# Kernel optimization log

Hardware: AMD Instinct MI355X
Metric: run time of the kernel (lower is better)

Reference implementation:

```python
import jax, jax.numpy as jnp
import numpy as np

B, S, D, H = 4, 2048, 1024, 16
HD = D // H  # head_dim = 64

def setup_inputs() -> dict:
    key = jax.random.key(0)
    ks = jax.random.split(key, 6)
    scale = 1.0 / np.sqrt(D)
    x = jax.random.normal(ks[0], (B, S, D), dtype=jnp.float32)
    Wq = jax.random.normal(ks[1], (D, D), dtype=jnp.float32) * scale
    Wk = jax.random.normal(ks[2], (D, D), dtype=jnp.float32) * scale
    Wv = jax.random.normal(ks[3], (D, D), dtype=jnp.float32) * scale
    Wo = jax.random.normal(ks[4], (D, D), dtype=jnp.float32) * scale
    z = jnp.zeros((D,), dtype=jnp.float32)
    return {"x": x, "Wq": Wq, "bq": z, "Wk": Wk, "bk": z, "Wv": Wv, "bv": z, "Wo": Wo, "bo": z}

def reference(x, Wq, bq, Wk, bk, Wv, bv, Wo, bo):
    b, s, d = x.shape
    hd = d // H
    def split_heads(t):
        return t.reshape(b, s, H, hd).swapaxes(1, 2)  # [B,H,S,hd]
    q = split_heads(x @ Wq + bq)
    k = split_heads(x @ Wk + bk)
    v = split_heads(x @ Wv + bv)
    logits = jnp.einsum('bhqd,bhkd->bhqk', q, k) / jnp.sqrt(jnp.asarray(hd, x.dtype))
    attn = jax.nn.softmax(logits, axis=-1)
    vals = jnp.einsum('bhqk,bhkd->bhqd', attn, v)
    vals = vals.swapaxes(1, 2).reshape(b, s, d)
    return vals @ Wo + bo
```

## Files before the change

kernel.cpp:

```cpp
#include <hip/hip_runtime.h>
#include <hip/hip_bf16.h>
#include <cstdint>
#include <cstddef>


typedef __attribute__((ext_vector_type(8))) short short8;
typedef __attribute__((ext_vector_type(8))) unsigned short ushort8;
typedef __attribute__((ext_vector_type(4))) unsigned short ushort4v;
typedef __attribute__((ext_vector_type(4))) float floatx4;

#define LOG2E 1.44269504088896340736f
#define QSCALE (0.125f * LOG2E)

__device__ __forceinline__ unsigned short f2bf(float f) {
  union { float f; unsigned int u; } c; c.f = f;
  return (unsigned short)((c.u + 0x7fffu + ((c.u >> 16) & 1u)) >> 16);
}

__device__ __forceinline__ unsigned int pack_bf16(float a, float b) {
  unsigned int ua = __builtin_bit_cast(unsigned int, a) + 0x8000u;
  unsigned int ub = __builtin_bit_cast(unsigned int, b) + 0x8000u;
  return __builtin_amdgcn_perm(ub, ua, 0x07060302);
}

__device__ __forceinline__ float fexp2(float x) {
#if __HIP_DEVICE_COMPILE__
  return __builtin_amdgcn_exp2f(x);
#else
  return x;
#endif
}

__device__ __forceinline__ void gl_lds16(const void* g, void* l) {
  __builtin_amdgcn_global_load_lds((__attribute__((address_space(1))) void*)g,
                                   (__attribute__((address_space(3))) void*)l, 16, 0, 0);
}

__global__ __launch_bounds__(256) void cast_x_kernel(const float* __restrict__ x,
                                                     unsigned short* __restrict__ xb, int n4) {
  int i = blockIdx.x * 256 + threadIdx.x;
  if (i >= n4) return;
  float4 v = ((const float4*)x)[i];
  ushort4v o;
  o.x = f2bf(v.x); o.y = f2bf(v.y); o.z = f2bf(v.z); o.w = f2bf(v.w);
  ((ushort4v*)xb)[i] = o;
}

__global__ __launch_bounds__(256) void transpose_w_kernel(
    const float* __restrict__ Wq, const float* __restrict__ Wk,
    const float* __restrict__ Wv, const float* __restrict__ Wo,
    unsigned short* __restrict__ Wqkv_t, unsigned short* __restrict__ Wo_t) {
  __shared__ float tile[32][33];
  const int which = blockIdx.z;
  const float* src = (which == 0) ? Wq : (which == 1) ? Wk : (which == 2) ? Wv : Wo;
  unsigned short* dst = (which == 3) ? Wo_t : (Wqkv_t + (size_t)which * 1024 * 1024);
  const int bn = blockIdx.x * 32;
  const int bk = blockIdx.y * 32;
  const int tx = threadIdx.x & 31, ty = threadIdx.x >> 5;
#pragma unroll
  for (int r = 0; r < 32; r += 8)
    tile[ty + r][tx] = src[(size_t)(bk + ty + r) * 1024 + bn + tx];
  __syncthreads();
#pragma unroll
  for (int r = 0; r < 32; r += 8)
    dst[(size_t)(bn + ty + r) * 1024 + bk + tx] = f2bf(tile[tx][ty + r]);
}

template <int MODE>
__global__ __launch_bounds__(256, 3) void gemm_bt(
    const unsigned short* __restrict__ A, const unsigned short* __restrict__ Bt,
    int M, int N, int K,
    const float* __restrict__ bias0, const float* __restrict__ bias1,
    const float* __restrict__ bias2,
    unsigned short* __restrict__ outQ, unsigned short* __restrict__ outK,
    unsigned short* __restrict__ outVt, float* __restrict__ outF) {
  __shared__ unsigned short As[128 * 32];
  __shared__ unsigned short Bs[128 * 32];

  const int tid = threadIdx.x;
  const int lane = tid & 63;
  const int wid = tid >> 6;
  const int wm = wid >> 1, wn = wid & 1;
  const int l15 = lane & 15, q4 = lane >> 4;
  const int bm = blockIdx.x * 128, bn = blockIdx.y * 128;

  const int rowL = lane >> 2;
  const int segL = (lane & 3) * 16;

  const char* Ab = (const char*)A;
  const char* Bb = (const char*)Bt;
  const size_t strideA = (size_t)K * 2;

  floatx4 acc[4][4] = {};

  for (int k0 = 0; k0 < K; k0 += 32) {
    __syncthreads();
#pragma unroll
    for (int c0 = 0; c0 < 2; ++c0) {
      const int c = wid * 2 + c0;
      gl_lds16(Ab + (size_t)(bm + c * 16 + rowL) * strideA + (size_t)k0 * 2 + segL,
               &As[c * 512]);
      gl_lds16(Bb + (size_t)(bn + c * 16 + rowL) * strideA + (size_t)k0 * 2 + segL,
               &Bs[c * 512]);
    }
    __syncthreads();

    short8 af[4], bfr[4];
#pragma unroll
    for (int i = 0; i < 4; ++i)
      af[i] = *(const short8*)&As[(wm * 64 + i * 16 + l15) * 32 + q4 * 8];
#pragma unroll
    for (int j = 0; j < 4; ++j)
      bfr[j] = *(const short8*)&Bs[(wn * 64 + j * 16 + l15) * 32 + q4 * 8];
#pragma unroll
    for (int i = 0; i < 4; ++i)
#pragma unroll
      for (int j = 0; j < 4; ++j)
        acc[i][j] = __builtin_amdgcn_mfma_f32_16x16x32_bf16(af[i], bfr[j], acc[i][j], 0, 0, 0);
  }

#pragma unroll
  for (int i = 0; i < 4; ++i) {
    const int row0 = bm + wm * 64 + i * 16 + q4 * 4;
#pragma unroll
    for (int j = 0; j < 4; ++j) {
      const int gn = bn + wn * 64 + j * 16 + l15;
      if (MODE == 0) {
        const int b = row0 >> 11, s0 = row0 & 2047;
        const int region = gn >> 10, d = gn & 1023;
        const int h = d >> 6, hd = d & 63;
        const size_t bh = (size_t)(b * 16 + h);
        if (region == 0) {
          const float bb = bias0[d];
#pragma unroll
          for (int r = 0; r < 4; ++r)
            outQ[(bh * 2048 + s0 + r) * 64 + hd] = f2bf((acc[i][j][r] + bb) * QSCALE);
        } else if (region == 1) {
          const float bb = bias1[d];
#pragma unroll
          for (int r = 0; r < 4; ++r)
            outK[(bh * 2048 + s0 + r) * 64 + hd] = f2bf(acc[i][j][r] + bb);
        } else {
          const float bb = bias2[d];
          ushort4v pk;
#pragma unroll
          for (int r = 0; r < 4; ++r) pk[r] = f2bf(acc[i][j][r] + bb);
          *(ushort4v*)&outVt[(bh * 64 + hd) * 2048 + s0] = pk;
        }
      } else {
        const float bb = bias0[gn];
#pragma unroll
        for (int r = 0; r < 4; ++r)
          outF[(size_t)(row0 + r) * N + gn] = acc[i][j][r] + bb;
      }
    }
  }
}

__global__ __launch_bounds__(256, 2) void flash_attn(
    const unsigned short* __restrict__ Q, const unsigned short* __restrict__ Kg,
    const unsigned short* __restrict__ Vt, unsigned short* __restrict__ Oout) {
  __shared__ unsigned short Ks[2][64 * 72];
  __shared__ unsigned short Vs[2][64 * 72];

  const int tid = threadIdx.x, lane = tid & 63, wid = tid >> 6;
  const int l15 = lane & 15, q4 = lane >> 4;
  const int bh = blockIdx.y;
  const int bb = bh >> 4, hh = bh & 15;
  const int q0 = blockIdx.x * 256;
  const size_t base = (size_t)bh * 2048 * 64;

  short8 qf[4][2];
#pragma unroll
  for (int s = 0; s < 4; ++s) {
    const unsigned short* qrow = Q + base + (size_t)(q0 + s * 64 + wid * 16 + l15) * 64;
    qf[s][0] = *(const short8*)(qrow + q4 * 8);
    qf[s][1] = *(const short8*)(qrow + 32 + q4 * 8);
  }

  const int sr = tid >> 2;
  const int sg = (tid & 3) * 16;
  const int loc = sr & 31;
  const int ph = (loc >> 4) & 1, pq = (loc >> 2) & 3, pr = loc & 3;
  const int gp = (sr & 32) + pq * 8 + ph * 4 + pr;
  const unsigned short* Kbase = Kg + base + (size_t)gp * 64 + sg;
  const unsigned short* Vbase = Vt + base + (size_t)sr * 2048 + sg;

  ushort8 kr0, kr1, vr0, vr1;
  kr0 = *(const ushort8*)Kbase;       kr1 = *(const ushort8*)(Kbase + 8);
  vr0 = *(const ushort8*)Vbase;       vr1 = *(const ushort8*)(Vbase + 8);
  *(ushort8*)&Ks[0][sr * 72 + sg] = kr0;  *(ushort8*)&Ks[0][sr * 72 + sg + 8] = kr1;
  *(ushort8*)&Vs[0][sr * 72 + sg] = vr0;  *(ushort8*)&Vs[0][sr * 72 + sg + 8] = vr1;
  kr0 = *(const ushort8*)(Kbase + 4096);  kr1 = *(const ushort8*)(Kbase + 4104);
  vr0 = *(const ushort8*)(Vbase + 64);    vr1 = *(const ushort8*)(Vbase + 72);

  floatx4 oacc[4][4] = {};
  float lsum[4] = {0.f, 0.f, 0.f, 0.f};

  for (int it = 0; it < 32; ++it) {
    const int cur = it & 1;
    __syncthreads();
    if (it < 31) {
      *(ushort8*)&Ks[cur ^ 1][sr * 72 + sg] = kr0;
      *(ushort8*)&Ks[cur ^ 1][sr * 72 + sg + 8] = kr1;
      *(ushort8*)&Vs[cur ^ 1][sr * 72 + sg] = vr0;
      *(ushort8*)&Vs[cur ^ 1][sr * 72 + sg + 8] = vr1;
    }
    if (it < 30) {
      const unsigned short* kp = Kbase + (size_t)(it + 2) * 4096;
      const unsigned short* vp = Vbase + (size_t)(it + 2) * 64;
      kr0 = *(const ushort8*)kp;       kr1 = *(const ushort8*)(kp + 8);
      vr0 = *(const ushort8*)vp;       vr1 = *(const ushort8*)(vp + 8);
    }

    short8 pf[4][2];
#pragma unroll
    for (int c = 0; c < 2; ++c) {
      floatx4 sc[4][2] = {};
#pragma unroll
      for (int tt = 0; tt < 2; ++tt) {
        const int t = 2 * c + tt;
        const unsigned short* krow = &Ks[cur][(t * 16 + l15) * 72];
        short8 kf0 = *(const short8*)(krow + q4 * 8);
        short8 kf1 = *(const short8*)(krow + 32 + q4 * 8);
#pragma unroll
        for (int s = 0; s < 4; ++s) {
          sc[s][tt] = __builtin_amdgcn_mfma_f32_16x16x32_bf16(kf0, qf[s][0], sc[s][tt], 0, 0, 0);
          sc[s][tt] = __builtin_amdgcn_mfma_f32_16x16x32_bf16(kf1, qf[s][1], sc[s][tt], 0, 0, 0);
        }
      }
#pragma unroll
      for (int s = 0; s < 4; ++s) {
        float e0 = fexp2(sc[s][0][0]), e1 = fexp2(sc[s][0][1]);
        float e2 = fexp2(sc[s][0][2]), e3 = fexp2(sc[s][0][3]);
        float e4 = fexp2(sc[s][1][0]), e5 = fexp2(sc[s][1][1]);
        float e6 = fexp2(sc[s][1][2]), e7 = fexp2(sc[s][1][3]);
        lsum[s] += ((e0 + e1) + (e2 + e3)) + ((e4 + e5) + (e6 + e7));
        union { unsigned int u[4]; short8 v; } cv;
        cv.u[0] = pack_bf16(e0, e1); cv.u[1] = pack_bf16(e2, e3);
        cv.u[2] = pack_bf16(e4, e5); cv.u[3] = pack_bf16(e6, e7);
        pf[s][c] = cv.v;
      }
    }

#pragma unroll
    for (int t = 0; t < 4; ++t) {
      const unsigned short* vrow = &Vs[cur][(t * 16 + l15) * 72 + q4 * 8];
      short8 vf0 = *(const short8*)vrow;
      short8 vf1 = *(const short8*)(vrow + 32);
#pragma unroll
      for (int s = 0; s < 4; ++s) {
        oacc[s][t] = __builtin_amdgcn_mfma_f32_16x16x32_bf16(vf0, pf[s][0], oacc[s][t], 0, 0, 0);
        oacc[s][t] = __builtin_amdgcn_mfma_f32_16x16x32_bf16(vf1, pf[s][1], oacc[s][t], 0, 0, 0);
      }
    }
  }

#pragma unroll
  for (int s = 0; s < 4; ++s) {
    float l = lsum[s];
    l += __shfl_xor(l, 16);
    l += __shfl_xor(l, 32);
    const float inv = 1.0f / l;
    const int srow = q0 + s * 64 + wid * 16 + l15;
    unsigned short* orow = Oout + ((size_t)bb * 2048 + srow) * 1024 + hh * 64;
#pragma unroll
    for (int t = 0; t < 4; ++t) {
      union { unsigned int u[2]; ushort4v s4; } cv;
      cv.u[0] = pack_bf16(oacc[s][t][0] * inv, oacc[s][t][1] * inv);
      cv.u[1] = pack_bf16(oacc[s][t][2] * inv, oacc[s][t][3] * inv);
      *(ushort4v*)(orow + t * 16 + q4 * 4) = cv.s4;
    }
  }
}

extern "C" void kernel_launch(void* const* d_in, const int* in_sizes, int n_in,
                              void* d_out, int out_size, void* d_ws, size_t ws_size,
                              hipStream_t stream) {
  const float* x  = (const float*)d_in[0];
  const float* Wq = (const float*)d_in[1];
  const float* bq = (const float*)d_in[2];
  const float* Wk = (const float*)d_in[3];
  const float* bk = (const float*)d_in[4];
  const float* Wv = (const float*)d_in[5];
  const float* bv = (const float*)d_in[6];
  const float* Wo = (const float*)d_in[7];
  const float* bo = (const float*)d_in[8];
  float* out = (float*)d_out;

  char* ws = (char*)d_ws;
  unsigned short* xb     = (unsigned short*)(ws);
  unsigned short* wqkv_t = (unsigned short*)(ws + (16u << 20));
  unsigned short* wo_t   = (unsigned short*)(ws + (22u << 20));
  unsigned short* Qb     = (unsigned short*)(ws + (24u << 20));
  unsigned short* Kb     = (unsigned short*)(ws + (40u << 20));
  unsigned short* Vtb    = (unsigned short*)(ws + (56u << 20));
  unsigned short* attn   = (unsigned short*)(ws + (72u << 20));
  (void)in_sizes; (void)n_in; (void)out_size; (void)ws_size;

  cast_x_kernel<<<dim3(8192), 256, 0, stream>>>(x, xb, 8192 * 1024 / 4);
  transpose_w_kernel<<<dim3(32, 32, 4), 256, 0, stream>>>(Wq, Wk, Wv, Wo, wqkv_t, wo_t);
  gemm_bt<0><<<dim3(64, 24), 256, 0, stream>>>(xb, wqkv_t, 8192, 3072, 1024,
                                               bq, bk, bv, Qb, Kb, Vtb, nullptr);
  flash_attn<<<dim3(8, 64), 256, 0, stream>>>(Qb, Kb, Vtb, attn);
  gemm_bt<1><<<dim3(64, 8), 256, 0, stream>>>(attn, wo_t, 8192, 1024, 1024,
                                              bo, nullptr, nullptr,
                                              nullptr, nullptr, nullptr, out);
}
```

Baseline: 273.3 us.

## Split flash attention over two KV halves and merge with a combine kernel

Attention now runs on a third grid dimension that splits the 2048-key sequence into two halves. Each block writes an unnormalized bf16 partial output and its row sums, and a new combine kernel adds the two halves and normalizes them into the attention layout. The goal is to double the number of blocks, and launch bounds are raised to 4 blocks per SM, so the GPU's compute units are better occupied. The cost is an extra kernel launch, extra global traffic for the partials, and some precision loss from storing the partials in bf16.

Result: slower. 813.7 us (+197.7%).

```diff
diff --git a/kernel.cpp b/kernel.cpp
--- a/kernel.cpp
+++ b/kernel.cpp
@@ -15,6 +15,10 @@
 __device__ __forceinline__ unsigned short f2bf(float f) {
   union { float f; unsigned int u; } c; c.f = f;
   return (unsigned short)((c.u + 0x7fffu + ((c.u >> 16) & 1u)) >> 16);
+}
+
+__device__ __forceinline__ float bf2f(unsigned short u) {
+  return __builtin_bit_cast(float, (unsigned int)u << 16);
 }
 
 __device__ __forceinline__ unsigned int pack_bf16(float a, float b) {
@@ -157,16 +161,17 @@
   }
 }
 
-__global__ __launch_bounds__(256, 2) void flash_attn(
+__global__ __launch_bounds__(256, 4) void flash_attn(
     const unsigned short* __restrict__ Q, const unsigned short* __restrict__ Kg,
-    const unsigned short* __restrict__ Vt, unsigned short* __restrict__ Oout) {
+    const unsigned short* __restrict__ Vt,
+    unsigned short* __restrict__ Opart, float* __restrict__ Lpart) {
   __shared__ unsigned short Ks[2][64 * 72];
   __shared__ unsigned short Vs[2][64 * 72];
 
   const int tid = threadIdx.x, lane = tid & 63, wid = tid >> 6;
   const int l15 = lane & 15, q4 = lane >> 4;
   const int bh = blockIdx.y;
-  const int bb = bh >> 4, hh = bh & 15;
+  const int z = blockIdx.z;
   const int q0 = blockIdx.x * 256;
   const size_t base = (size_t)bh * 2048 * 64;
 
@@ -183,8 +188,8 @@
   const int loc = sr & 31;
   const int ph = (loc >> 4) & 1, pq = (loc >> 2) & 3, pr = loc & 3;
   const int gp = (sr & 32) + pq * 8 + ph * 4 + pr;
-  const unsigned short* Kbase = Kg + base + (size_t)gp * 64 + sg;
-  const unsigned short* Vbase = Vt + base + (size_t)sr * 2048 + sg;
+  const unsigned short* Kbase = Kg + base + (size_t)z * 16 * 4096 + (size_t)gp * 64 + sg;
+  const unsigned short* Vbase = Vt + base + (size_t)z * 1024 + (size_t)sr * 2048 + sg;
 
   ushort8 kr0, kr1, vr0, vr1;
   kr0 = *(const ushort8*)Kbase;       kr1 = *(const ushort8*)(Kbase + 8);
@@ -197,16 +202,16 @@
   floatx4 oacc[4][4] = {};
   float lsum[4] = {0.f, 0.f, 0.f, 0.f};
 
-  for (int it = 0; it < 32; ++it) {
+  for (int it = 0; it < 16; ++it) {
     const int cur = it & 1;
     __syncthreads();
-    if (it < 31) {
+    if (it < 15) {
       *(ushort8*)&Ks[cur ^ 1][sr * 72 + sg] = kr0;
       *(ushort8*)&Ks[cur ^ 1][sr * 72 + sg + 8] = kr1;
       *(ushort8*)&Vs[cur ^ 1][sr * 72 + sg] = vr0;
       *(ushort8*)&Vs[cur ^ 1][sr * 72 + sg + 8] = vr1;
     }
-    if (it < 30) {
+    if (it < 14) {
       const unsigned short* kp = Kbase + (size_t)(it + 2) * 4096;
       const unsigned short* vp = Vbase + (size_t)(it + 2) * 64;
       kr0 = *(const ushort8*)kp;       kr1 = *(const ushort8*)(kp + 8);
@@ -256,22 +261,46 @@
     }
   }
 
+  const size_t zb = ((size_t)z * 64 + bh);
 #pragma unroll
   for (int s = 0; s < 4; ++s) {
     float l = lsum[s];
     l += __shfl_xor(l, 16);
     l += __shfl_xor(l, 32);
-    const float inv = 1.0f / l;
     const int srow = q0 + s * 64 + wid * 16 + l15;
-    unsigned short* orow = Oout + ((size_t)bb * 2048 + srow) * 1024 + hh * 64;
+    if (q4 == 0) Lpart[zb * 2048 + srow] = l;
+    unsigned short* orow = Opart + (zb * 2048 + srow) * 64;
 #pragma unroll
     for (int t = 0; t < 4; ++t) {
       union { unsigned int u[2]; ushort4v s4; } cv;
-      cv.u[0] = pack_bf16(oacc[s][t][0] * inv, oacc[s][t][1] * inv);
-      cv.u[1] = pack_bf16(oacc[s][t][2] * inv, oacc[s][t][3] * inv);
+      cv.u[0] = pack_bf16(oacc[s][t][0], oacc[s][t][1]);
+      cv.u[1] = pack_bf16(oacc[s][t][2], oacc[s][t][3]);
       *(ushort4v*)(orow + t * 16 + q4 * 4) = cv.s4;
     }
   }
+}
+
+__global__ __launch_bounds__(256) void combine_attn(
+    const unsigned short* __restrict__ Opart, const float* __restrict__ Lpart,
+    unsigned short* __restrict__ attn) {
+  const int c = blockIdx.x * 256 + threadIdx.x;
+  const int bh = c >> 14;
+  const int rem = c & 16383;
+  const int s = rem >> 3;
+  const int seg = rem & 7;
+  const size_t o1 = ((size_t)bh * 2048 + s) * 64 + seg * 8;
+  const size_t o2 = o1 + (size_t)64 * 2048 * 64;
+  const float inv = 1.0f / (Lpart[bh * 2048 + s] + Lpart[64 * 2048 + bh * 2048 + s]);
+  const ushort8 a = *(const ushort8*)&Opart[o1];
+  const ushort8 b = *(const ushort8*)&Opart[o2];
+  float f[8];
+#pragma unroll
+  for (int i = 0; i < 8; ++i) f[i] = (bf2f(a[i]) + bf2f(b[i])) * inv;
+  union { unsigned int u[4]; ushort8 v; } cv;
+  cv.u[0] = pack_bf16(f[0], f[1]); cv.u[1] = pack_bf16(f[2], f[3]);
+  cv.u[2] = pack_bf16(f[4], f[5]); cv.u[3] = pack_bf16(f[6], f[7]);
+  const int b_ = bh >> 4, h = bh & 15;
+  *(ushort8*)&attn[((size_t)b_ * 2048 + s) * 1024 + h * 64 + seg * 8] = cv.v;
 }
 
 extern "C" void kernel_launch(void* const* d_in, const int* in_sizes, int n_in,
@@ -296,13 +325,16 @@
   unsigned short* Kb     = (unsigned short*)(ws + (40u << 20));
   unsigned short* Vtb    = (unsigned short*)(ws + (56u << 20));
   unsigned short* attn   = (unsigned short*)(ws + (72u << 20));
+  unsigned short* Opart  = (unsigned short*)(ws + (88u << 20));
+  float*          Lpart  = (float*)(ws + (120u << 20));
   (void)in_sizes; (void)n_in; (void)out_size; (void)ws_size;
 
   cast_x_kernel<<<dim3(8192), 256, 0, stream>>>(x, xb, 8192 * 1024 / 4);
   transpose_w_kernel<<<dim3(32, 32, 4), 256, 0, stream>>>(Wq, Wk, Wv, Wo, wqkv_t, wo_t);
   gemm_bt<0><<<dim3(64, 24), 256, 0, stream>>>(xb, wqkv_t, 8192, 3072, 1024,
                                                bq, bk, bv, Qb, Kb, Vtb, nullptr);
-  flash_attn<<<dim3(8, 64), 256, 0, stream>>>(Qb, Kb, Vtb, attn);
+  flash_attn<<<dim3(8, 64, 2), 256, 0, stream>>>(Qb, Kb, Vtb, Opart, Lpart);
+  combine_attn<<<dim3(4096), 256, 0, stream>>>(Opart, Lpart, attn);
   gemm_bt<1><<<dim3(64, 8), 256, 0, stream>>>(attn, wo_t, 8192, 1024, 1024,
                                               bo, nullptr, nullptr,
                                               nullptr, nullptr, nullptr, out);
```
